# Performance work log

Measured on AMD Instinct MI355X. Metric: run time of the kernel, lower is better.

Reference implementation:

```python
import jax, jax.numpy as jnp
import numpy as np

B, E, R, A, NV, SEL = 512, 1024, 1024, 512, 196, 36

def _lstm_cell(x, h, c, Wih, bih, Whh, bhh):
    g = x @ Wih.T + bih + h @ Whh.T + bhh
    i, f, gg, o = jnp.split(g, 4, axis=1)  # torch gate order i,f,g,o
    c2 = jax.nn.sigmoid(f) * c + jax.nn.sigmoid(i) * jnp.tanh(gg)
    h2 = jax.nn.sigmoid(o) * jnp.tanh(c2)
    return h2, c2

def _attention(h, feats, p_feats, Wh, bh, Wa, ba):
    # feats: [B,S,R], p_feats: [B,S,A]
    att_h = h @ Wh.T + bh                       # [B,A]
    dot = jnp.tanh(p_feats + att_h[:, None, :])  # [B,S,A]
    scores = jnp.einsum('bsa,a->bs', dot, Wa[0]) + ba[0]
    w = jax.nn.softmax(scores, axis=1)
    return jnp.einsum('bs,bsd->bd', w, feats)

def setup_inputs() -> dict:
    key = jax.random.key(0)
    ks = jax.random.split(key, 32)
    s = 0.02
    inp = {
        'xt': jax.random.normal(ks[0], (B, E), jnp.float32),
        'fc_feats': jax.random.normal(ks[1], (B, R), jnp.float32),
        'att_feats': jax.random.normal(ks[2], (B, NV, R), jnp.float32),
        'p_att_feats': jax.random.normal(ks[3], (B, NV, A), jnp.float32),
        'state_h': jax.random.normal(ks[4], (2, B, R), jnp.float32),
        'state_c': jax.random.normal(ks[5], (2, B, R), jnp.float32),
        # att_lstm: input E + 2R
        'W_ih_att': jax.random.normal(ks[6], (4 * R, E + 2 * R), jnp.float32) * s,
        'b_ih_att': jnp.zeros((4 * R,), jnp.float32),
        'W_hh_att': jax.random.normal(ks[7], (4 * R, R), jnp.float32) * s,
        'b_hh_att': jnp.zeros((4 * R,), jnp.float32),
        # lang_lstm: input 3R
        'W_ih_lang': jax.random.normal(ks[8], (4 * R, 3 * R), jnp.float32) * s,
        'b_ih_lang': jnp.zeros((4 * R,), jnp.float32),
        'W_hh_lang': jax.random.normal(ks[9], (4 * R, R), jnp.float32) * s,
        'b_hh_lang': jnp.zeros((4 * R,), jnp.float32),
        # attention 1
        'Wh2att1': jax.random.normal(ks[10], (A, R), jnp.float32) * s,
        'bh2att1': jnp.zeros((A,), jnp.float32),
        'Walpha1': jax.random.normal(ks[11], (1, A), jnp.float32) * s,
        'balpha1': jnp.zeros((1,), jnp.float32),
        # vf attention
        'Wh2att2': jax.random.normal(ks[12], (A, R), jnp.float32) * s,
        'bh2att2': jnp.zeros((A,), jnp.float32),
        'Walpha2': jax.random.normal(ks[13], (1, A), jnp.float32) * s,
        'balpha2': jnp.zeros((1,), jnp.float32),
        # vf_layer and p_vf
        'W_vf': jax.random.normal(ks[14], (NV, 2 * R), jnp.float32) * s,
        'b_vf': jnp.zeros((NV,), jnp.float32),
        'W_pvf': jax.random.normal(ks[15], (A, R), jnp.float32) * s,
        'b_pvf': jnp.zeros((A,), jnp.float32),
    }
    return inp

def reference(xt, fc_feats, att_feats, p_att_feats, state_h, state_c,
              W_ih_att, b_ih_att, W_hh_att, b_hh_att,
              W_ih_lang, b_ih_lang, W_hh_lang, b_hh_lang,
              Wh2att1, bh2att1, Walpha1, balpha1,
              Wh2att2, bh2att2, Walpha2, balpha2,
              W_vf, b_vf, W_pvf, b_pvf):
    # dropout in eval mode -> identity
    prev_h = state_h[-1]
    att_lstm_input = jnp.concatenate([prev_h, fc_feats, xt], axis=1)
    h_att, c_att = _lstm_cell(att_lstm_input, state_h[0], state_c[0],
                              W_ih_att, b_ih_att, W_hh_att, b_hh_att)
    att = _attention(h_att, att_feats, p_att_feats, Wh2att1, bh2att1, Walpha1, balpha1)
    conc = jnp.concatenate([att, h_att], axis=1)          # [B,2R]
    vf_ha = conc @ W_vf.T + b_vf                          # [B,NV]
    vf_soft = jax.nn.softmax(vf_ha, axis=1)
    _, vf_ix = jax.lax.top_k(vf_soft, SEL)                # [B,SEL] (descending)
    arr1 = jnp.take_along_axis(att_feats, vf_ix[:, :, None], axis=1)  # [B,SEL,R]
    p_vf_feats = arr1 @ W_pvf.T + b_pvf                   # [B,SEL,A]
    vf_att = _attention(h_att, arr1, p_vf_feats, Wh2att2, bh2att2, Walpha2, balpha2)
    lang_lstm_input = jnp.concatenate([vf_att, h_att, att], axis=1)
    h_lang, c_lang = _lstm_cell(lang_lstm_input, state_h[1], state_c[1],
                                W_ih_lang, b_ih_lang, W_hh_lang, b_hh_lang)
    output = h_lang
    new_h = jnp.stack([h_att, h_lang])
    new_c = jnp.stack([c_att, c_lang])
    return output, new_h, new_c
```

## Files before the change

kernel.cpp:

```cpp
#include <hip/hip_runtime.h>

typedef __attribute__((ext_vector_type(4))) float f32x4;
typedef __attribute__((ext_vector_type(8))) _Float16 half8;
typedef __attribute__((ext_vector_type(4))) _Float16 half4;

__device__ __forceinline__ float fast_tanh(float x) {
  float e = __expf(2.f * x);
  return 1.f - 2.f / (e + 1.f);
}
__device__ __forceinline__ float fast_sigmoid(float x) {
  return 1.f / (1.f + __expf(-x));
}

__device__ __forceinline__ void gl_lds16(const _Float16* g, _Float16* l) {
  __builtin_amdgcn_global_load_lds(
      (const __attribute__((address_space(1))) void*)g,
      (__attribute__((address_space(3))) void*)l, 16, 0, 0);
}

template<int SPLIT, int OUT16>
__global__ __launch_bounds__(512, 2) void gemm_big(
    const _Float16* __restrict__ Ahp, const _Float16* __restrict__ Alp,
    const _Float16* __restrict__ Bhp, const _Float16* __restrict__ Blp,
    int K, int Kc, void* __restrict__ Cp, long czstride)
{
  __shared__ _Float16 sAh[2][512 * 32];
  __shared__ _Float16 sBh[2][64 * 32];
  __shared__ _Float16 sAl[SPLIT == 3 ? 2 : 1][SPLIT == 3 ? 512 * 32 : 8];
  __shared__ _Float16 sBl[SPLIT == 3 ? 2 : 1][SPLIT == 3 ? 64 * 32 : 8];

  const int lane = threadIdx.x & 63, wid = threadIdx.x >> 6;
  const int sr = lane >> 2;
  const int sgr = (lane & 3) ^ ((lane >> 3) & 3);
  const int l16 = lane & 15, k8 = lane >> 4;
  const int koff = ((k8 ^ ((lane >> 1) & 3))) * 8;

  const int  z     = blockIdx.x;
  const long nbase = (long)blockIdx.y * 64;
  const int  kt0   = z * Kc;

  f32x4 acc[4][4];
#pragma unroll
  for (int i = 0; i < 4; i++)
#pragma unroll
    for (int j = 0; j < 4; j++) acc[i][j] = (f32x4){0.f, 0.f, 0.f, 0.f};

  auto STAGE = [&](int buf, int kt) {
#pragma unroll
    for (int g = 0; g < 4; g++) {
      const int rloc = wid * 64 + g * 16 + sr;
      gl_lds16(Ahp + (long)rloc * K + kt + sgr * 8, &sAh[buf][(wid * 64 + g * 16) * 32]);
      if (SPLIT == 3)
        gl_lds16(Alp + (long)rloc * K + kt + sgr * 8, &sAl[buf][(wid * 64 + g * 16) * 32]);
    }
    if (wid < 4) {
      const int rloc = wid * 16 + sr;
      gl_lds16(Bhp + (nbase + rloc) * K + kt + sgr * 8, &sBh[buf][(wid * 16) * 32]);
    } else if (SPLIT == 3) {
      const int rloc = (wid - 4) * 16 + sr;
      gl_lds16(Blp + (nbase + rloc) * K + kt + sgr * 8, &sBl[buf][((wid - 4) * 16) * 32]);
    }
  };

  STAGE(0, kt0);
  __syncthreads();

  int buf = 0;
  const int nst = Kc >> 5;
  for (int t = 0; t < nst; t++) {
    if (t + 1 < nst) STAGE(buf ^ 1, kt0 + (t + 1) * 32);

    half8 ah[4], bh[4];
#pragma unroll
    for (int m = 0; m < 4; m++)
      ah[m] = *(const half8*)&sAh[buf][(wid * 64 + m * 16 + l16) * 32 + koff];
#pragma unroll
    for (int n = 0; n < 4; n++)
      bh[n] = *(const half8*)&sBh[buf][(n * 16 + l16) * 32 + koff];
#pragma unroll
    for (int m = 0; m < 4; m++)
#pragma unroll
      for (int n = 0; n < 4; n++)
        acc[m][n] = __builtin_amdgcn_mfma_f32_16x16x32_f16(ah[m], bh[n], acc[m][n], 0, 0, 0);
    if (SPLIT == 3) {
      half8 al[4], bl[4];
#pragma unroll
      for (int m = 0; m < 4; m++)
        al[m] = *(const half8*)&sAl[buf][(wid * 64 + m * 16 + l16) * 32 + koff];
#pragma unroll
      for (int n = 0; n < 4; n++)
        bl[n] = *(const half8*)&sBl[buf][(n * 16 + l16) * 32 + koff];
#pragma unroll
      for (int m = 0; m < 4; m++)
#pragma unroll
        for (int n = 0; n < 4; n++) {
          acc[m][n] = __builtin_amdgcn_mfma_f32_16x16x32_f16(al[m], bh[n], acc[m][n], 0, 0, 0);
          acc[m][n] = __builtin_amdgcn_mfma_f32_16x16x32_f16(ah[m], bl[n], acc[m][n], 0, 0, 0);
        }
    }
    __syncthreads();
    buf ^= 1;
  }

  const long czoff = (long)z * czstride;
#pragma unroll
  for (int m = 0; m < 4; m++)
#pragma unroll
    for (int n = 0; n < 4; n++) {
      const long row0 = wid * 64 + m * 16 + (lane >> 4) * 4;
      const long col  = nbase + n * 16 + l16;
#pragma unroll
      for (int j = 0; j < 4; j++) {
        const long idx = czoff + (row0 + j) * 4096 + col;
        if (OUT16) ((_Float16*)Cp)[idx] = (_Float16)acc[m][n][j];
        else       ((float*)Cp)[idx] = acc[m][n][j];
      }
    }
}

template<int SPLIT, int OUT16, int NGUARD, int SWAPXY>
__global__ __launch_bounds__(256) void gemm16(
    const _Float16* __restrict__ Ahp, const _Float16* __restrict__ Alp, int lda,
    const _Float16* __restrict__ Bhp, const _Float16* __restrict__ Blp, int ldb,
    void* __restrict__ Cp, int ldc, long czstride,
    int N, int Kc)
{
  __shared__ _Float16 sAh[128 * 32];
  __shared__ _Float16 sBh[128 * 32];
  __shared__ _Float16 sAl[SPLIT == 3 ? 128 * 32 : 8];
  __shared__ _Float16 sBl[SPLIT == 3 ? 128 * 32 : 8];

  const int tid = threadIdx.x, lane = tid & 63, wid = tid >> 6;
  const int wm = wid >> 1, wn = wid & 1;
  const int l16 = lane & 15, k8 = lane >> 4;
  const int sr = lane >> 2;
  const int scol = ((lane & 3) ^ ((lane >> 3) & 3)) * 8;
  const int koff = ((k8 ^ ((lane >> 1) & 3))) * 8;

  const int  kt0   = blockIdx.z * Kc;
  const long abase = (long)(SWAPXY ? blockIdx.x : blockIdx.y) * 128;
  const long bbase = (long)(SWAPXY ? blockIdx.y : blockIdx.x) * 128;

  const int r0 = wid * 32 + sr;
  const int r1 = wid * 32 + 16 + sr;
  long br0 = bbase + r0, br1 = bbase + r1;
  if (NGUARD) {
    if (br0 > N - 1) br0 = N - 1;
    if (br1 > N - 1) br1 = N - 1;
  }

  const _Float16* ga0 = Ahp + (abase + r0) * (long)lda + kt0 + scol;
  const _Float16* ga1 = Ahp + (abase + r1) * (long)lda + kt0 + scol;
  const _Float16* gb0 = Bhp + br0 * (long)ldb + kt0 + scol;
  const _Float16* gb1 = Bhp + br1 * (long)ldb + kt0 + scol;
  const _Float16* la0 = SPLIT == 3 ? Alp + (abase + r0) * (long)lda + kt0 + scol : nullptr;
  const _Float16* la1 = SPLIT == 3 ? Alp + (abase + r1) * (long)lda + kt0 + scol : nullptr;
  const _Float16* lb0 = SPLIT == 3 ? Blp + br0 * (long)ldb + kt0 + scol : nullptr;
  const _Float16* lb1 = SPLIT == 3 ? Blp + br1 * (long)ldb + kt0 + scol : nullptr;

  const int e0 = (wid * 32) * 32;
  const int e1 = (wid * 32 + 16) * 32;

  f32x4 acc[4][4];
#pragma unroll
  for (int i = 0; i < 4; i++)
#pragma unroll
    for (int j = 0; j < 4; j++) acc[i][j] = (f32x4){0.f, 0.f, 0.f, 0.f};

  for (int kk = 0; kk < Kc; kk += 32) {
    gl_lds16(ga0 + kk, sAh + e0);
    gl_lds16(ga1 + kk, sAh + e1);
    gl_lds16(gb0 + kk, sBh + e0);
    gl_lds16(gb1 + kk, sBh + e1);
    if (SPLIT == 3) {
      gl_lds16(la0 + kk, sAl + e0);
      gl_lds16(la1 + kk, sAl + e1);
      gl_lds16(lb0 + kk, sBl + e0);
      gl_lds16(lb1 + kk, sBl + e1);
    }
    __syncthreads();

    half8 ah[4], bh[4];
#pragma unroll
    for (int m = 0; m < 4; m++)
      ah[m] = *(const half8*)&sAh[(wm * 64 + m * 16 + l16) * 32 + koff];
#pragma unroll
    for (int n = 0; n < 4; n++)
      bh[n] = *(const half8*)&sBh[(wn * 64 + n * 16 + l16) * 32 + koff];
#pragma unroll
    for (int m = 0; m < 4; m++)
#pragma unroll
      for (int n = 0; n < 4; n++)
        acc[m][n] = __builtin_amdgcn_mfma_f32_16x16x32_f16(ah[m], bh[n], acc[m][n], 0, 0, 0);
    if (SPLIT == 3) {
      half8 al[4], bl[4];
#pragma unroll
      for (int m = 0; m < 4; m++)
        al[m] = *(const half8*)&sAl[(wm * 64 + m * 16 + l16) * 32 + koff];
#pragma unroll
      for (int n = 0; n < 4; n++)
        bl[n] = *(const half8*)&sBl[(wn * 64 + n * 16 + l16) * 32 + koff];
#pragma unroll
      for (int m = 0; m < 4; m++)
#pragma unroll
        for (int n = 0; n < 4; n++) {
          acc[m][n] = __builtin_amdgcn_mfma_f32_16x16x32_f16(al[m], bh[n], acc[m][n], 0, 0, 0);
          acc[m][n] = __builtin_amdgcn_mfma_f32_16x16x32_f16(ah[m], bl[n], acc[m][n], 0, 0, 0);
        }
    }
    __syncthreads();
  }

  const long czoff = (long)blockIdx.z * czstride;
#pragma unroll
  for (int m = 0; m < 4; m++)
#pragma unroll
    for (int n = 0; n < 4; n++) {
      const long row0 = abase + wm * 64 + m * 16 + (lane >> 4) * 4;
      const long col  = bbase + wn * 64 + n * 16 + l16;
      if (!NGUARD || col < N) {
#pragma unroll
        for (int j = 0; j < 4; j++) {
          const long idx = (row0 + j) * (long)ldc + col + czoff;
          if (OUT16) ((_Float16*)Cp)[idx] = (_Float16)acc[m][n][j];
          else       ((float*)Cp)[idx] = acc[m][n][j];
        }
      }
    }
}

__global__ __launch_bounds__(256) void pack_kernel(
    const float* __restrict__ xt, const float* __restrict__ fc,
    const float* __restrict__ sh,
    _Float16* __restrict__ X1h, _Float16* __restrict__ X1l)
{
  int i = blockIdx.x * 256 + threadIdx.x;
  int b = i >> 10, rr = i & 1023;
  long base = (long)b * 4096;
  float v[4];
  v[0] = sh[524288 + i];
  v[1] = fc[i];
  v[2] = xt[i];
  v[3] = sh[i];
#pragma unroll
  for (int j = 0; j < 4; j++) {
    _Float16 h = (_Float16)v[j];
    X1h[base + j * 1024 + rr] = h;
    X1l[base + j * 1024 + rr] = (_Float16)(v[j] - (float)h);
  }
}

__global__ __launch_bounds__(256) void convertA_kernel(
    const float* __restrict__ WihA, const float* __restrict__ WhhA,
    const float* __restrict__ Wh1, const float* __restrict__ Wh2,
    const float* __restrict__ Wvf, const float* __restrict__ Wpvf,
    _Float16* __restrict__ WcAh, _Float16* __restrict__ WcAl,
    _Float16* __restrict__ W12h, _Float16* __restrict__ Wvfh,
    _Float16* __restrict__ Wvfl, _Float16* __restrict__ Wpvfh)
{
  int bi = blockIdx.x, t = threadIdx.x;
  if (bi < 16384) {
    long e = ((long)bi * 256 + t) * 4;
    int row = (int)(e >> 12), col = (int)(e & 4095);
    const float* src = (col < 3072) ? WihA + (long)row * 3072 + col
                                    : WhhA + (long)row * 1024 + (col - 3072);
    f32x4 v = *(const f32x4*)src;
    half4 h, l;
#pragma unroll
    for (int j = 0; j < 4; j++) { h[j] = (_Float16)v[j]; l[j] = (_Float16)(v[j] - (float)h[j]); }
    *(half4*)&WcAh[e] = h;
    *(half4*)&WcAl[e] = l;
  } else if (bi < 17408) {
    long e = ((long)(bi - 16384) * 256 + t) * 4;
    int row = (int)(e >> 10), col = (int)(e & 1023);
    const float* src = (row < 512) ? Wh1 + (long)row * 1024 + col
                                   : Wh2 + (long)(row - 512) * 1024 + col;
    f32x4 v = *(const f32x4*)src;
    half4 h;
#pragma unroll
    for (int j = 0; j < 4; j++) h[j] = (_Float16)v[j];
    *(half4*)&W12h[e] = h;
  } else if (bi < 17800) {
    long e = ((long)(bi - 17408) * 256 + t) * 4;
    f32x4 v = *(const f32x4*)(Wvf + e);
    half4 h, l;
#pragma unroll
    for (int j = 0; j < 4; j++) { h[j] = (_Float16)v[j]; l[j] = (_Float16)(v[j] - (float)h[j]); }
    *(half4*)&Wvfh[e] = h;
    *(half4*)&Wvfl[e] = l;
  } else {
    long e = ((long)(bi - 17800) * 256 + t) * 4;
    f32x4 v = *(const f32x4*)(Wpvf + e);
    half4 h;
#pragma unroll
    for (int j = 0; j < 4; j++) h[j] = (_Float16)v[j];
    *(half4*)&Wpvfh[e] = h;
  }
}

__global__ __launch_bounds__(256) void convertL_kernel(
    const float* __restrict__ WihL, const float* __restrict__ WhhL,
    _Float16* __restrict__ WcLh)
{
  long e = ((long)blockIdx.x * 256 + threadIdx.x) * 4;
  int row = (int)(e >> 12), col = (int)(e & 4095);
  const float* src = (col < 3072) ? WihL + (long)row * 3072 + col
                                  : WhhL + (long)row * 1024 + (col - 3072);
  f32x4 v = *(const f32x4*)src;
  half4 h;
#pragma unroll
  for (int j = 0; j < 4; j++) h[j] = (_Float16)v[j];
  *(half4*)&WcLh[e] = h;
}

template<int NP, bool H16, bool ATT>
__global__ __launch_bounds__(256) void lstm_act_kernel(
    const void* __restrict__ gp, const float* __restrict__ bih,
    const float* __restrict__ bhh, const float* __restrict__ cin,
    float* __restrict__ hOut, float* __restrict__ cOut,
    _Float16* __restrict__ hatt_h, _Float16* __restrict__ conch,
    _Float16* __restrict__ concl, float* __restrict__ hOut2)
{
  const long S = 2097152;
  int i = blockIdx.x * 256 + threadIdx.x;
  int b = i >> 10, rr = i & 1023;
  long gb = (long)b * 4096;
  float g4[4];
#pragma unroll
  for (int q = 0; q < 4; q++) {
    float s = 0.f;
#pragma unroll
    for (int z = 0; z < NP; z++) {
      long off = (long)z * S + gb + q * 1024 + rr;
      s += H16 ? (float)((const _Float16*)gp)[off] : ((const float*)gp)[off];
    }
    g4[q] = s + bih[q * 1024 + rr] + bhh[q * 1024 + rr];
  }
  float c  = cin[i];
  float c2 = fast_sigmoid(g4[1]) * c + fast_sigmoid(g4[0]) * fast_tanh(g4[2]);
  float h2 = fast_sigmoid(g4[3]) * fast_tanh(c2);
  hOut[i] = h2;
  cOut[i] = c2;
  if (hOut2) hOut2[i] = h2;
  if (ATT) {
    _Float16 hh = (_Float16)h2;
    hatt_h[i] = hh;
    conch[(long)b * 2048 + 1024 + rr] = hh;
    concl[(long)b * 2048 + 1024 + rr] = (_Float16)(h2 - (float)hh);
  }
}

__global__ __launch_bounds__(256) void x2fill_kernel(
    const float* __restrict__ hatt, const float* __restrict__ sh,
    _Float16* __restrict__ x2h)
{
  int i = blockIdx.x * 256 + threadIdx.x;
  int b = i >> 10, rr = i & 1023;
  x2h[(long)b * 4096 + 1024 + rr] = (_Float16)hatt[i];
  x2h[(long)b * 4096 + 3072 + rr] = (_Float16)sh[524288 + i];
}

__global__ __launch_bounds__(256) void reduce_atth_kernel(
    const float* __restrict__ p, float* __restrict__ o)
{
  int i = (blockIdx.x * 256 + threadIdx.x) * 4;
  f32x4 a = *(const f32x4*)(p + i);
  f32x4 b = *(const f32x4*)(p + 524288 + i);
  f32x4 c = *(const f32x4*)(p + 1048576 + i);
  f32x4 d = *(const f32x4*)(p + 1572864 + i);
  *(f32x4*)(o + i) = a + b + c + d;
}

__global__ __launch_bounds__(256) void score1_kernel(
    const float* __restrict__ pf, const float* __restrict__ atth,
    const float* __restrict__ bh,
    const float* __restrict__ walpha, const float* __restrict__ balpha,
    float* __restrict__ out, int nrows)
{
  int gw = blockIdx.x * 4 + (threadIdx.x >> 6);
  int lane = threadIdx.x & 63;
  if (gw >= nrows) return;
  int b = gw / 196;
  const float* p  = pf + (long)gw * 512 + lane * 8;
  const float* ah = atth + (long)b * 1024 + lane * 8;
  const float* bp = bh + lane * 8;
  const float* wp = walpha + lane * 8;
  float acc = 0.f;
#pragma unroll
  for (int u = 0; u < 2; u++) {
    f32x4 pv = *(const f32x4*)(p + u * 4);
    f32x4 av = *(const f32x4*)(ah + u * 4);
    f32x4 bv = *(const f32x4*)(bp + u * 4);
    f32x4 wv = *(const f32x4*)(wp + u * 4);
#pragma unroll
    for (int j = 0; j < 4; j++)
      acc += fast_tanh(pv[j] + av[j] + bv[j]) * wv[j];
  }
#pragma unroll
  for (int off = 32; off; off >>= 1) acc += __shfl_xor(acc, off);
  if (lane == 0) out[gw] = acc + balpha[0];
}

__global__ __launch_bounds__(256) void attsum1_kernel(
    const float* __restrict__ scores, const float* __restrict__ feats,
    _Float16* __restrict__ conch, _Float16* __restrict__ concl, _Float16* __restrict__ x2h)
{
  __shared__ float w[256];
  int b = blockIdx.x, t = threadIdx.x;
  float s0 = (t < 196) ? scores[b * 196 + t] : -3.0e38f;
  w[t] = s0;
  __syncthreads();
  float mx = -3.0e38f;
  for (int i = 0; i < 196; i++) mx = fmaxf(mx, w[i]);
  float sum = 0.f;
  for (int i = 0; i < 196; i++) sum += __expf(w[i] - mx);
  float inv = 1.f / sum;
  __syncthreads();
  if (t < 196) w[t] = __expf(s0 - mx) * inv;
  __syncthreads();
  f32x4 acc = (f32x4){0.f, 0.f, 0.f, 0.f};
  const float* fb = feats + (long)b * 200704 + t * 4;
  for (int s0i = 0; s0i < 192; s0i += 8) {
    f32x4 v[8];
#pragma unroll
    for (int u = 0; u < 8; u++) v[u] = *(const f32x4*)(fb + (long)(s0i + u) * 1024);
#pragma unroll
    for (int u = 0; u < 8; u++) {
      float ws = w[s0i + u];
#pragma unroll
      for (int j = 0; j < 4; j++) acc[j] += ws * v[u][j];
    }
  }
#pragma unroll
  for (int u = 192; u < 196; u++) {
    float ws = w[u];
    f32x4 v = *(const f32x4*)(fb + (long)u * 1024);
#pragma unroll
    for (int j = 0; j < 4; j++) acc[j] += ws * v[j];
  }
  half4 h, l;
#pragma unroll
  for (int j = 0; j < 4; j++) { h[j] = (_Float16)acc[j]; l[j] = (_Float16)(acc[j] - (float)h[j]); }
  *(half4*)&conch[(long)b * 2048 + t * 4] = h;
  *(half4*)&concl[(long)b * 2048 + t * 4] = l;
  *(half4*)&x2h[(long)b * 4096 + 2048 + t * 4] = h;
}

__global__ __launch_bounds__(256) void vfatt_kernel(
    const _Float16* __restrict__ pvf16, const float* __restrict__ atth2,
    const float* __restrict__ bh2att2, const float* __restrict__ b_pvf,
    const float* __restrict__ walpha2, const float* __restrict__ balpha2,
    const _Float16* __restrict__ arr1h, _Float16* __restrict__ x2h)
{
  __shared__ float w[40];
  int b = blockIdx.x, tid = threadIdx.x;
  int lane = tid & 63, wv = tid >> 6;

  float add[8], wal[8];
#pragma unroll
  for (int u = 0; u < 8; u++) {
    int a = lane * 8 + u;
    add[u] = atth2[(long)b * 1024 + a] + bh2att2[a] + b_pvf[a];
    wal[u] = walpha2[a];
  }
  for (int j = wv; j < 36; j += 4) {
    half8 hv = *(const half8*)&pvf16[((long)b * 36 + j) * 512 + lane * 8];
    float acc = 0.f;
#pragma unroll
    for (int u = 0; u < 8; u++)
      acc += fast_tanh((float)hv[u] + add[u]) * wal[u];
#pragma unroll
    for (int off = 32; off; off >>= 1) acc += __shfl_xor(acc, off);
    if (lane == 0) w[j] = acc + balpha2[0];
  }
  __syncthreads();
  float mx = -3.0e38f;
  for (int i = 0; i < 36; i++) mx = fmaxf(mx, w[i]);
  float sum = 0.f;
  for (int i = 0; i < 36; i++) sum += __expf(w[i] - mx);
  float inv = 1.f / sum;
  __syncthreads();
  if (tid < 36) w[tid] = __expf(w[tid] - mx) * inv;
  __syncthreads();
  f32x4 acc = (f32x4){0.f, 0.f, 0.f, 0.f};
  const _Float16* fb = arr1h + (long)b * 36 * 1024 + tid * 4;
#pragma unroll 4
  for (int s = 0; s < 36; s++) {
    float ws = w[s];
    half4 v = *(const half4*)(fb + (long)s * 1024);
#pragma unroll
    for (int j = 0; j < 4; j++) acc[j] += ws * (float)v[j];
  }
  half4 h;
#pragma unroll
  for (int j = 0; j < 4; j++) h[j] = (_Float16)acc[j];
  *(half4*)&x2h[(long)b * 4096 + tid * 4] = h;
}

template<int NP>
__global__ __launch_bounds__(64) void topk_kernel(
    const float* __restrict__ vfp, const float* __restrict__ b_vf, int* __restrict__ ix)
{
  int b = blockIdx.x;
  int lane = threadIdx.x;
  float v[4];
#pragma unroll
  for (int j = 0; j < 4; j++) {
    int s = lane + 64 * j;
    float sum = -3.0e38f;
    if (s < 196) {
      sum = b_vf[s];
#pragma unroll
      for (int z = 0; z < NP; z++) sum += vfp[(long)z * 100352 + b * 196 + s];
    }
    v[j] = sum;
  }
  for (int it = 0; it < 36; it++) {
    float bv = -3.0e38f; int bs = 1 << 20;
#pragma unroll
    for (int j = 0; j < 4; j++) {
      int s = lane + 64 * j;
      if (v[j] > bv) { bv = v[j]; bs = s; }
    }
#pragma unroll
    for (int off = 32; off; off >>= 1) {
      float ov = __shfl_xor(bv, off);
      int   os = __shfl_xor(bs, off);
      if (ov > bv || (ov == bv && os < bs)) { bv = ov; bs = os; }
    }
    if ((bs & 63) == lane) v[bs >> 6] = -3.0e38f;
    if (lane == 0) ix[b * 36 + it] = bs;
  }
}

__global__ __launch_bounds__(256) void gather_conv_kernel(
    const float* __restrict__ feats, const int* __restrict__ ix, _Float16* __restrict__ dst)
{
  int bj = blockIdx.x;
  int b = bj / 36;
  int s = ix[bj];
  int t = threadIdx.x;
  f32x4 v = *(const f32x4*)(feats + ((long)b * 196 + s) * 1024 + t * 4);
  half4 h;
#pragma unroll
  for (int j = 0; j < 4; j++) h[j] = (_Float16)v[j];
  *(half4*)&dst[(long)bj * 1024 + t * 4] = h;
}

extern "C" void kernel_launch(void* const* d_in, const int* in_sizes, int n_in,
                              void* d_out, int out_size, void* d_ws, size_t ws_size,
                              hipStream_t stream) {
  const float* xt        = (const float*)d_in[0];
  const float* fc_feats  = (const float*)d_in[1];
  const float* att_feats = (const float*)d_in[2];
  const float* p_att     = (const float*)d_in[3];
  const float* state_h   = (const float*)d_in[4];
  const float* state_c   = (const float*)d_in[5];
  const float* b_ih_att  = (const float*)d_in[7];
  const float* b_hh_att  = (const float*)d_in[9];
  const float* b_ih_lang = (const float*)d_in[11];
  const float* b_hh_lang = (const float*)d_in[13];
  const float* bh2att1   = (const float*)d_in[15];
  const float* Walpha1   = (const float*)d_in[16];
  const float* balpha1   = (const float*)d_in[17];
  const float* bh2att2   = (const float*)d_in[19];
  const float* Walpha2   = (const float*)d_in[20];
  const float* balpha2   = (const float*)d_in[21];
  const float* b_vf      = (const float*)d_in[23];
  const float* b_pvf     = (const float*)d_in[25];

  float* out = (float*)d_out;
  float* W = (float*)d_ws;

  _Float16* WcAh   = (_Float16*)(W + 0);
  _Float16* WcAl   = (_Float16*)(W + 8388608);
  _Float16* X1h    = (_Float16*)(W + 16777216);
  _Float16* X1l    = (_Float16*)(W + 17825792);
  float*    g1p    = W + 18874368;
  _Float16* hatt_h = (_Float16*)(W + 27262976);
  _Float16* W12h   = (_Float16*)(W + 27525120);
  _Float16* Wvfh   = (_Float16*)(W + 28049408);
  _Float16* Wvfl   = (_Float16*)(W + 28250112);
  _Float16* Wpvfh  = (_Float16*)(W + 28450816);
  _Float16* WcLh   = WcAh;
  float*    vfhap  = W + 8388608;
  _Float16* arr1h  = (_Float16*)(W + 8388608);
  _Float16* g2ph   = (_Float16*)(W + 8388608);
  _Float16* conch  = (_Float16*)(W + 17825792);
  _Float16* concl  = (_Float16*)(W + 18350080);
  int*      vfix   = (int*)(W + 17825792);
  float*    atthp  = W + 18874368;
  float*    atth   = W + 20971520;
  _Float16* X2h    = (_Float16*)(W + 21495808);
  float*    scores1= W + 22544384;
  _Float16* pvf16  = (_Float16*)(W + 22544384);

  float* out_h0 = out + 524288;
  float* out_h1 = out + 2 * 524288;
  float* out_c0 = out + 3 * 524288;
  float* out_c1 = out + 4 * 524288;

  pack_kernel<<<2048, 256, 0, stream>>>(xt, fc_feats, state_h, X1h, X1l);

  convertA_kernel<<<18312, 256, 0, stream>>>(
      (const float*)d_in[6], (const float*)d_in[8],
      (const float*)d_in[14], (const float*)d_in[18],
      (const float*)d_in[22], (const float*)d_in[24],
      WcAh, WcAl, W12h, Wvfh, Wvfl, Wpvfh);

  gemm_big<3, 0><<<dim3(4, 64), 512, 0, stream>>>(
      X1h, X1l, WcAh, WcAl, 4096, 1024, g1p, 2097152);

  convertL_kernel<<<16384, 256, 0, stream>>>(
      (const float*)d_in[10], (const float*)d_in[12], WcLh);

  lstm_act_kernel<4, false, true><<<2048, 256, 0, stream>>>(
      g1p, b_ih_att, b_hh_att, state_c, out_h0, out_c0,
      hatt_h, conch, concl, nullptr);

  x2fill_kernel<<<2048, 256, 0, stream>>>(out_h0, state_h, X2h);

  gemm16<1, 0, 0, 0><<<dim3(8, 4, 4), 256, 0, stream>>>(
      hatt_h, nullptr, 1024, W12h, nullptr, 1024, atthp, 1024, 524288, 1024, 256);
  reduce_atth_kernel<<<512, 256, 0, stream>>>(atthp, atth);

  score1_kernel<<<25088, 256, 0, stream>>>(
      p_att, atth, bh2att1, Walpha1, balpha1, scores1, 100352);

  attsum1_kernel<<<512, 256, 0, stream>>>(scores1, att_feats, conch, concl, X2h);

  gemm16<3, 0, 1, 0><<<dim3(2, 4, 16), 256, 0, stream>>>(
      conch, concl, 2048, Wvfh, Wvfl, 2048, vfhap, 196, 100352, 196, 128);

  topk_kernel<16><<<512, 64, 0, stream>>>(vfhap, b_vf, vfix);

  gather_conv_kernel<<<18432, 256, 0, stream>>>(att_feats, vfix, arr1h);

  gemm16<1, 1, 0, 1><<<dim3(144, 4, 1), 256, 0, stream>>>(
      arr1h, nullptr, 1024, Wpvfh, nullptr, 1024, pvf16, 512, 0, 512, 1024);

  vfatt_kernel<<<512, 256, 0, stream>>>(
      pvf16, atth + 512, bh2att2, b_pvf, Walpha2, balpha2, arr1h, X2h);

  gemm_big<1, 1><<<dim3(4, 64), 512, 0, stream>>>(
      X2h, nullptr, WcLh, nullptr, 4096, 1024, g2ph, 2097152);

  lstm_act_kernel<4, true, false><<<2048, 256, 0, stream>>>(
      g2ph, b_ih_lang, b_hh_lang, state_c + 524288, out, out_c1,
      nullptr, nullptr, nullptr, out_h1);
}
```

Baseline: 466.4 us.

## Double-buffer gemm16, replace gemm_big with it, fuse x2fill into LSTM activation

Adds double-buffered LDS staging to gemm16, with explicit vmcnt waits and raw s_barrier so the global-to-LDS loads for the next k-tile overlap the MFMA work on the current one. Removes the gemm_big kernel and runs both large LSTM GEMMs through gemm16 on a 128x128 tile grid of 32x4x4 blocks. Folds the x2fill kernel into lstm_act so one launch and one reread of h_att are dropped. Gives the workspace buffers disjoint regions, so the lang weights no longer overwrite the att weights and they can be converted in parallel. This uses more LDS per block, and the hand-written waitcnt counts must exactly match the number of issued loads.

```diff
diff --git a/kernel.cpp b/kernel.cpp
--- a/kernel.cpp
+++ b/kernel.cpp
@@ -16,106 +16,6 @@
   __builtin_amdgcn_global_load_lds(
       (const __attribute__((address_space(1))) void*)g,
       (__attribute__((address_space(3))) void*)l, 16, 0, 0);
-}
-
-template<int SPLIT, int OUT16>
-__global__ __launch_bounds__(512, 2) void gemm_big(
-    const _Float16* __restrict__ Ahp, const _Float16* __restrict__ Alp,
-    const _Float16* __restrict__ Bhp, const _Float16* __restrict__ Blp,
-    int K, int Kc, void* __restrict__ Cp, long czstride)
-{
-  __shared__ _Float16 sAh[2][512 * 32];
-  __shared__ _Float16 sBh[2][64 * 32];
-  __shared__ _Float16 sAl[SPLIT == 3 ? 2 : 1][SPLIT == 3 ? 512 * 32 : 8];
-  __shared__ _Float16 sBl[SPLIT == 3 ? 2 : 1][SPLIT == 3 ? 64 * 32 : 8];
-
-  const int lane = threadIdx.x & 63, wid = threadIdx.x >> 6;
-  const int sr = lane >> 2;
-  const int sgr = (lane & 3) ^ ((lane >> 3) & 3);
-  const int l16 = lane & 15, k8 = lane >> 4;
-  const int koff = ((k8 ^ ((lane >> 1) & 3))) * 8;
-
-  const int  z     = blockIdx.x;
-  const long nbase = (long)blockIdx.y * 64;
-  const int  kt0   = z * Kc;
-
-  f32x4 acc[4][4];
-#pragma unroll
-  for (int i = 0; i < 4; i++)
-#pragma unroll
-    for (int j = 0; j < 4; j++) acc[i][j] = (f32x4){0.f, 0.f, 0.f, 0.f};
-
-  auto STAGE = [&](int buf, int kt) {
-#pragma unroll
-    for (int g = 0; g < 4; g++) {
-      const int rloc = wid * 64 + g * 16 + sr;
-      gl_lds16(Ahp + (long)rloc * K + kt + sgr * 8, &sAh[buf][(wid * 64 + g * 16) * 32]);
-      if (SPLIT == 3)
-        gl_lds16(Alp + (long)rloc * K + kt + sgr * 8, &sAl[buf][(wid * 64 + g * 16) * 32]);
-    }
-    if (wid < 4) {
-      const int rloc = wid * 16 + sr;
-      gl_lds16(Bhp + (nbase + rloc) * K + kt + sgr * 8, &sBh[buf][(wid * 16) * 32]);
-    } else if (SPLIT == 3) {
-      const int rloc = (wid - 4) * 16 + sr;
-      gl_lds16(Blp + (nbase + rloc) * K + kt + sgr * 8, &sBl[buf][((wid - 4) * 16) * 32]);
-    }
-  };
-
-  STAGE(0, kt0);
-  __syncthreads();
-
-  int buf = 0;
-  const int nst = Kc >> 5;
-  for (int t = 0; t < nst; t++) {
-    if (t + 1 < nst) STAGE(buf ^ 1, kt0 + (t + 1) * 32);
-
-    half8 ah[4], bh[4];
-#pragma unroll
-    for (int m = 0; m < 4; m++)
-      ah[m] = *(const half8*)&sAh[buf][(wid * 64 + m * 16 + l16) * 32 + koff];
-#pragma unroll
-    for (int n = 0; n < 4; n++)
-      bh[n] = *(const half8*)&sBh[buf][(n * 16 + l16) * 32 + koff];
-#pragma unroll
-    for (int m = 0; m < 4; m++)
-#pragma unroll
-      for (int n = 0; n < 4; n++)
-        acc[m][n] = __builtin_amdgcn_mfma_f32_16x16x32_f16(ah[m], bh[n], acc[m][n], 0, 0, 0);
-    if (SPLIT == 3) {
-      half8 al[4], bl[4];
-#pragma unroll
-      for (int m = 0; m < 4; m++)
-        al[m] = *(const half8*)&sAl[buf][(wid * 64 + m * 16 + l16) * 32 + koff];
-#pragma unroll
-      for (int n = 0; n < 4; n++)
-        bl[n] = *(const half8*)&sBl[buf][(n * 16 + l16) * 32 + koff];
-#pragma unroll
-      for (int m = 0; m < 4; m++)
-#pragma unroll
-        for (int n = 0; n < 4; n++) {
-          acc[m][n] = __builtin_amdgcn_mfma_f32_16x16x32_f16(al[m], bh[n], acc[m][n], 0, 0, 0);
-          acc[m][n] = __builtin_amdgcn_mfma_f32_16x16x32_f16(ah[m], bl[n], acc[m][n], 0, 0, 0);
-        }
-    }
-    __syncthreads();
-    buf ^= 1;
-  }
-
-  const long czoff = (long)z * czstride;
-#pragma unroll
-  for (int m = 0; m < 4; m++)
-#pragma unroll
-    for (int n = 0; n < 4; n++) {
-      const long row0 = wid * 64 + m * 16 + (lane >> 4) * 4;
-      const long col  = nbase + n * 16 + l16;
-#pragma unroll
-      for (int j = 0; j < 4; j++) {
-        const long idx = czoff + (row0 + j) * 4096 + col;
-        if (OUT16) ((_Float16*)Cp)[idx] = (_Float16)acc[m][n][j];
-        else       ((float*)Cp)[idx] = acc[m][n][j];
-      }
-    }
 }
 
 template<int SPLIT, int OUT16, int NGUARD, int SWAPXY>
@@ -125,10 +25,10 @@
     void* __restrict__ Cp, int ldc, long czstride,
     int N, int Kc)
 {
-  __shared__ _Float16 sAh[128 * 32];
-  __shared__ _Float16 sBh[128 * 32];
-  __shared__ _Float16 sAl[SPLIT == 3 ? 128 * 32 : 8];
-  __shared__ _Float16 sBl[SPLIT == 3 ? 128 * 32 : 8];
+  __shared__ _Float16 sAh[2][128 * 32];
+  __shared__ _Float16 sBh[2][128 * 32];
+  __shared__ _Float16 sAl[SPLIT == 3 ? 2 : 1][SPLIT == 3 ? 128 * 32 : 8];
+  __shared__ _Float16 sBl[SPLIT == 3 ? 2 : 1][SPLIT == 3 ? 128 * 32 : 8];
 
   const int tid = threadIdx.x, lane = tid & 63, wid = tid >> 6;
   const int wm = wid >> 1, wn = wid & 1;
@@ -167,26 +67,42 @@
 #pragma unroll
     for (int j = 0; j < 4; j++) acc[i][j] = (f32x4){0.f, 0.f, 0.f, 0.f};
 
-  for (int kk = 0; kk < Kc; kk += 32) {
-    gl_lds16(ga0 + kk, sAh + e0);
-    gl_lds16(ga1 + kk, sAh + e1);
-    gl_lds16(gb0 + kk, sBh + e0);
-    gl_lds16(gb1 + kk, sBh + e1);
+  auto STAGE = [&](int buf, int kk) {
+    gl_lds16(ga0 + kk, &sAh[buf][e0]);
+    gl_lds16(ga1 + kk, &sAh[buf][e1]);
+    gl_lds16(gb0 + kk, &sBh[buf][e0]);
+    gl_lds16(gb1 + kk, &sBh[buf][e1]);
     if (SPLIT == 3) {
-      gl_lds16(la0 + kk, sAl + e0);
-      gl_lds16(la1 + kk, sAl + e1);
-      gl_lds16(lb0 + kk, sBl + e0);
-      gl_lds16(lb1 + kk, sBl + e1);
-    }
-    __syncthreads();
+      gl_lds16(la0 + kk, &sAl[buf][e0]);
+      gl_lds16(la1 + kk, &sAl[buf][e1]);
+      gl_lds16(lb0 + kk, &sBl[buf][e0]);
+      gl_lds16(lb1 + kk, &sBl[buf][e1]);
+    }
+  };
+
+  STAGE(0, 0);
+
+  const int nst = Kc >> 5;
+  for (int t = 0; t < nst; t++) {
+    const int buf = t & 1;
+    if (t + 1 < nst) {
+      STAGE(buf ^ 1, (t + 1) * 32);
+      if (SPLIT == 3) asm volatile("s_waitcnt vmcnt(8)" ::: "memory");
+      else            asm volatile("s_waitcnt vmcnt(4)" ::: "memory");
+    } else {
+      asm volatile("s_waitcnt vmcnt(0)" ::: "memory");
+    }
+    __builtin_amdgcn_sched_barrier(0);
+    __builtin_amdgcn_s_barrier();
+    __builtin_amdgcn_sched_barrier(0);
 
     half8 ah[4], bh[4];
 #pragma unroll
     for (int m = 0; m < 4; m++)
-      ah[m] = *(const half8*)&sAh[(wm * 64 + m * 16 + l16) * 32 + koff];
+      ah[m] = *(const half8*)&sAh[buf][(wm * 64 + m * 16 + l16) * 32 + koff];
 #pragma unroll
     for (int n = 0; n < 4; n++)
-      bh[n] = *(const half8*)&sBh[(wn * 64 + n * 16 + l16) * 32 + koff];
+      bh[n] = *(const half8*)&sBh[buf][(wn * 64 + n * 16 + l16) * 32 + koff];
 #pragma unroll
     for (int m = 0; m < 4; m++)
 #pragma unroll
@@ -196,10 +112,10 @@
       half8 al[4], bl[4];
 #pragma unroll
       for (int m = 0; m < 4; m++)
-        al[m] = *(const half8*)&sAl[(wm * 64 + m * 16 + l16) * 32 + koff];
+        al[m] = *(const half8*)&sAl[buf][(wm * 64 + m * 16 + l16) * 32 + koff];
 #pragma unroll
       for (int n = 0; n < 4; n++)
-        bl[n] = *(const half8*)&sBl[(wn * 64 + n * 16 + l16) * 32 + koff];
+        bl[n] = *(const half8*)&sBl[buf][(wn * 64 + n * 16 + l16) * 32 + koff];
 #pragma unroll
       for (int m = 0; m < 4; m++)
 #pragma unroll
@@ -208,7 +124,9 @@
           acc[m][n] = __builtin_amdgcn_mfma_f32_16x16x32_f16(ah[m], bl[n], acc[m][n], 0, 0, 0);
         }
     }
-    __syncthreads();
+    __builtin_amdgcn_sched_barrier(0);
+    __builtin_amdgcn_s_barrier();
+    __builtin_amdgcn_sched_barrier(0);
   }
 
   const long czoff = (long)blockIdx.z * czstride;
@@ -319,7 +237,8 @@
     const float* __restrict__ bhh, const float* __restrict__ cin,
     float* __restrict__ hOut, float* __restrict__ cOut,
     _Float16* __restrict__ hatt_h, _Float16* __restrict__ conch,
-    _Float16* __restrict__ concl, float* __restrict__ hOut2)
+    _Float16* __restrict__ concl, _Float16* __restrict__ x2h,
+    const float* __restrict__ sh, float* __restrict__ hOut2)
 {
   const long S = 2097152;
   int i = blockIdx.x * 256 + threadIdx.x;
@@ -347,17 +266,9 @@
     hatt_h[i] = hh;
     conch[(long)b * 2048 + 1024 + rr] = hh;
     concl[(long)b * 2048 + 1024 + rr] = (_Float16)(h2 - (float)hh);
-  }
-}
-
-__global__ __launch_bounds__(256) void x2fill_kernel(
-    const float* __restrict__ hatt, const float* __restrict__ sh,
-    _Float16* __restrict__ x2h)
-{
-  int i = blockIdx.x * 256 + threadIdx.x;
-  int b = i >> 10, rr = i & 1023;
-  x2h[(long)b * 4096 + 1024 + rr] = (_Float16)hatt[i];
-  x2h[(long)b * 4096 + 3072 + rr] = (_Float16)sh[524288 + i];
+    x2h[(long)b * 4096 + 1024 + rr] = hh;
+    x2h[(long)b * 4096 + 3072 + rr] = (_Float16)sh[524288 + i];
+  }
 }
 
 __global__ __launch_bounds__(256) void reduce_atth_kernel(
@@ -574,26 +485,26 @@
 
   _Float16* WcAh   = (_Float16*)(W + 0);
   _Float16* WcAl   = (_Float16*)(W + 8388608);
-  _Float16* X1h    = (_Float16*)(W + 16777216);
-  _Float16* X1l    = (_Float16*)(W + 17825792);
-  float*    g1p    = W + 18874368;
-  _Float16* hatt_h = (_Float16*)(W + 27262976);
-  _Float16* W12h   = (_Float16*)(W + 27525120);
-  _Float16* Wvfh   = (_Float16*)(W + 28049408);
-  _Float16* Wvfl   = (_Float16*)(W + 28250112);
-  _Float16* Wpvfh  = (_Float16*)(W + 28450816);
-  _Float16* WcLh   = WcAh;
-  float*    vfhap  = W + 8388608;
-  _Float16* arr1h  = (_Float16*)(W + 8388608);
-  _Float16* g2ph   = (_Float16*)(W + 8388608);
-  _Float16* conch  = (_Float16*)(W + 17825792);
-  _Float16* concl  = (_Float16*)(W + 18350080);
-  int*      vfix   = (int*)(W + 17825792);
-  float*    atthp  = W + 18874368;
-  float*    atth   = W + 20971520;
-  _Float16* X2h    = (_Float16*)(W + 21495808);
-  float*    scores1= W + 22544384;
-  _Float16* pvf16  = (_Float16*)(W + 22544384);
+  _Float16* WcLh   = (_Float16*)(W + 16777216);
+  _Float16* X1h    = (_Float16*)(W + 25165824);
+  _Float16* X1l    = (_Float16*)(W + 26214400);
+  float*    g1p    = W + 27262976;
+  _Float16* hatt_h = (_Float16*)(W + 35651584);
+  _Float16* W12h   = (_Float16*)(W + 35913728);
+  _Float16* Wvfh   = (_Float16*)(W + 36438016);
+  _Float16* Wvfl   = (_Float16*)(W + 36638720);
+  _Float16* Wpvfh  = (_Float16*)(W + 36839424);
+  float*    atthp  = W + 37101568;
+  float*    atth   = W + 39198720;
+  _Float16* conch  = (_Float16*)(W + 39723008);
+  _Float16* concl  = (_Float16*)(W + 40247296);
+  _Float16* X2h    = (_Float16*)(W + 40771584);
+  float*    scores1= W + 41820160;
+  float*    vfhap  = W + 41920512;
+  int*      vfix   = (int*)(W + 43526144);
+  _Float16* arr1h  = (_Float16*)(W + 43544576);
+  _Float16* pvf16  = (_Float16*)(W + 52981760);
+  _Float16* g2ph   = (_Float16*)(W + 57700352);
 
   float* out_h0 = out + 524288;
   float* out_h1 = out + 2 * 524288;
@@ -608,17 +519,15 @@
       (const float*)d_in[22], (const float*)d_in[24],
       WcAh, WcAl, W12h, Wvfh, Wvfl, Wpvfh);
 
-  gemm_big<3, 0><<<dim3(4, 64), 512, 0, stream>>>(
-      X1h, X1l, WcAh, WcAl, 4096, 1024, g1p, 2097152);
+  gemm16<3, 0, 0, 0><<<dim3(32, 4, 4), 256, 0, stream>>>(
+      X1h, X1l, 4096, WcAh, WcAl, 4096, g1p, 4096, 2097152, 4096, 1024);
 
   convertL_kernel<<<16384, 256, 0, stream>>>(
       (const float*)d_in[10], (const float*)d_in[12], WcLh);
 
   lstm_act_kernel<4, false, true><<<2048, 256, 0, stream>>>(
       g1p, b_ih_att, b_hh_att, state_c, out_h0, out_c0,
-      hatt_h, conch, concl, nullptr);
-
-  x2fill_kernel<<<2048, 256, 0, stream>>>(out_h0, state_h, X2h);
+      hatt_h, conch, concl, X2h, state_h, nullptr);
 
   gemm16<1, 0, 0, 0><<<dim3(8, 4, 4), 256, 0, stream>>>(
       hatt_h, nullptr, 1024, W12h, nullptr, 1024, atthp, 1024, 524288, 1024, 256);
@@ -642,10 +551,10 @@
   vfatt_kernel<<<512, 256, 0, stream>>>(
       pvf16, atth + 512, bh2att2, b_pvf, Walpha2, balpha2, arr1h, X2h);
 
-  gemm_big<1, 1><<<dim3(4, 64), 512, 0, stream>>>(
-      X2h, nullptr, WcLh, nullptr, 4096, 1024, g2ph, 2097152);
+  gemm16<1, 1, 0, 0><<<dim3(32, 4, 4), 256, 0, stream>>>(
+      X2h, nullptr, 4096, WcLh, nullptr, 4096, g2ph, 4096, 2097152, 4096, 1024);
 
   lstm_act_kernel<4, true, false><<<2048, 256, 0, stream>>>(
       g2ph, b_ih_lang, b_hh_lang, state_c + 524288, out, out_c1,
-      nullptr, nullptr, nullptr, out_h1);
-}
+      nullptr, nullptr, nullptr, nullptr, nullptr, out_h1);
+}
```

Result: faster. 411.9 us (-11.7%).
